# Kernel optimization log

Measured on AMD Instinct MI355X. Metric: run time of the kernel, lower is better.

## Reference

```python
import jax, jax.numpy as jnp
import numpy as np

N = 128          # batch size
C = 1000         # num_classes
NUM_DATA = 50000 # dataset size


def setup_inputs() -> dict:
    key = jax.random.key(0)
    k1, k2, k3 = jax.random.split(key, 3)
    outputs = jax.random.normal(k1, (N, C), dtype=jnp.float32)
    # label_confidence = train_givenY / rowsum(train_givenY): rows sum to 1
    conf = jax.random.uniform(k2, (NUM_DATA, C), dtype=jnp.float32)
    conf = conf / conf.sum(axis=1, keepdims=True)
    index = jax.random.randint(k3, (N,), 0, NUM_DATA, dtype=jnp.int64)
    return {"outputs": outputs, "label_confidence": conf, "index": index}


def reference(outputs, label_confidence, index):
    # softmax over classes: [N, C]
    p = jax.nn.softmax(outputs, axis=1)
    eye = jnp.eye(C, dtype=p.dtype)
    # |softmax broadcast vs one-hot|, summed over last dim -> [N, C]
    # (materializes [N, C, C] like the torch original)
    loss = jnp.abs(p[:, None, :] - eye[None, :, :]).sum(axis=-1)
    conf = label_confidence[index]          # [N, C]
    return (loss * conf).sum(axis=1).mean()
```

## Files before the change

kernel.cpp:

```cpp
#include <hip/hip_runtime.h>


#define NROWS 128
#define NCLS  1000

__global__ __launch_bounds__(256) void row_loss_kernel(
    const float* __restrict__ outputs,
    const float* __restrict__ conf,
    const int*   __restrict__ index,
    float* __restrict__ ws)
{
    const int row  = blockIdx.x;
    const int tid  = threadIdx.x;
    const int lane = tid & 63;
    const int wave = tid >> 6;

    __shared__ float redm[4];
    __shared__ float rz[4], rd[4], rs[4];
    __shared__ float bmax;

    const int j = tid * 4;
    float4 o = make_float4(-INFINITY, -INFINITY, -INFINITY, -INFINITY);
    if (j < NCLS) {
        o = *reinterpret_cast<const float4*>(outputs + (size_t)row * NCLS + j);
    }

    float m = fmaxf(fmaxf(o.x, o.y), fmaxf(o.z, o.w));
    #pragma unroll
    for (int off = 32; off > 0; off >>= 1)
        m = fmaxf(m, __shfl_down(m, off, 64));
    if (lane == 0) redm[wave] = m;
    __syncthreads();
    if (tid == 0)
        bmax = fmaxf(fmaxf(redm[0], redm[1]), fmaxf(redm[2], redm[3]));
    __syncthreads();
    m = bmax;

    float z = 0.f, dot = 0.f, sc = 0.f;
    if (j < NCLS) {
        const float* crow = conf + (size_t)index[row] * NCLS;
        const float4 cf = *reinterpret_cast<const float4*>(crow + j);
        const float e0 = __expf(o.x - m);
        const float e1 = __expf(o.y - m);
        const float e2 = __expf(o.z - m);
        const float e3 = __expf(o.w - m);
        z   = (e0 + e1) + (e2 + e3);
        dot = e0 * cf.x + e1 * cf.y + e2 * cf.z + e3 * cf.w;
        sc  = (cf.x + cf.y) + (cf.z + cf.w);
    }
    #pragma unroll
    for (int off = 32; off > 0; off >>= 1) {
        z   += __shfl_down(z,   off, 64);
        dot += __shfl_down(dot, off, 64);
        sc  += __shfl_down(sc,  off, 64);
    }
    if (lane == 0) { rz[wave] = z; rd[wave] = dot; rs[wave] = sc; }
    __syncthreads();
    if (tid == 0) {
        const float Z = (rz[0] + rz[1]) + (rz[2] + rz[3]);
        const float D = (rd[0] + rd[1]) + (rd[2] + rd[3]);
        const float S = (rs[0] + rs[1]) + (rs[2] + rs[3]);
        ws[row] = 2.f * S - 2.f * D / Z;
    }
}

__global__ __launch_bounds__(128) void final_reduce_kernel(
    const float* __restrict__ ws, float* __restrict__ out)
{
    const int tid = threadIdx.x;
    float v = ws[tid];
    #pragma unroll
    for (int off = 32; off > 0; off >>= 1)
        v += __shfl_down(v, off, 64);
    __shared__ float r[2];
    if ((tid & 63) == 0) r[tid >> 6] = v;
    __syncthreads();
    if (tid == 0) out[0] = (r[0] + r[1]) * (1.0f / (float)NROWS);
}

extern "C" void kernel_launch(void* const* d_in, const int* in_sizes, int n_in,
                              void* d_out, int out_size, void* d_ws, size_t ws_size,
                              hipStream_t stream) {
    const float* outputs = (const float*)d_in[0];
    const float* conf    = (const float*)d_in[1];
    const int*   index   = (const int*)d_in[2];
    float* out = (float*)d_out;
    float* ws  = (float*)d_ws;

    row_loss_kernel<<<NROWS, 256, 0, stream>>>(outputs, conf, index, ws);
    final_reduce_kernel<<<1, 128, 0, stream>>>(ws, out);
}
```

Before: 229.4 us.

## Fuse row loss and final reduction into a single-block wave-per-row kernel

Replaces the two-kernel design (128 blocks computing per-row loss, then a reduction kernel) with one 1024-thread block in which each wave processes eight rows using wave-level xor shuffles, then reduces per-wave sums in shared memory. This removes the second launch, the workspace round trip and the block-level barriers for row max. In exchange, all work runs on a single CU, so memory bandwidth and latency hiding are limited to one compute unit for roughly 1 MB of reads.

Result: slower. 249.0 us (+8.6%).

```diff
diff --git a/kernel.cpp b/kernel.cpp
--- a/kernel.cpp
+++ b/kernel.cpp
@@ -3,79 +3,82 @@
 
 #define NROWS 128
 #define NCLS  1000
+#define NF4   250
 
-__global__ __launch_bounds__(256) void row_loss_kernel(
+__global__ __launch_bounds__(1024) void fused_loss_kernel(
     const float* __restrict__ outputs,
     const float* __restrict__ conf,
     const int*   __restrict__ index,
-    float* __restrict__ ws)
+    float* __restrict__ out)
 {
-    const int row  = blockIdx.x;
     const int tid  = threadIdx.x;
     const int lane = tid & 63;
     const int wave = tid >> 6;
 
-    __shared__ float redm[4];
-    __shared__ float rz[4], rd[4], rs[4];
-    __shared__ float bmax;
+    int idxs[8];
+    #pragma unroll
+    for (int i = 0; i < 8; ++i) idxs[i] = index[wave + 16 * i];
 
-    const int j = tid * 4;
-    float4 o = make_float4(-INFINITY, -INFINITY, -INFINITY, -INFINITY);
-    if (j < NCLS) {
-        o = *reinterpret_cast<const float4*>(outputs + (size_t)row * NCLS + j);
+    float acc = 0.f;
+
+    #pragma unroll
+    for (int i = 0; i < 8; ++i) {
+        const int row = wave + 16 * i;
+        const float* orow = outputs + (size_t)row * NCLS;
+        const float* crow = conf + (size_t)idxs[i] * NCLS;
+
+        float4 o[4], c[4];
+        #pragma unroll
+        for (int k = 0; k < 4; ++k) {
+            const int p = lane + 64 * k;
+            o[k] = (p < NF4) ? reinterpret_cast<const float4*>(orow)[p]
+                             : make_float4(-INFINITY, -INFINITY, -INFINITY, -INFINITY);
+        }
+        #pragma unroll
+        for (int k = 0; k < 4; ++k) {
+            const int p = lane + 64 * k;
+            c[k] = (p < NF4) ? reinterpret_cast<const float4*>(crow)[p]
+                             : make_float4(0.f, 0.f, 0.f, 0.f);
+        }
+
+        float m = -INFINITY;
+        #pragma unroll
+        for (int k = 0; k < 4; ++k)
+            m = fmaxf(m, fmaxf(fmaxf(o[k].x, o[k].y), fmaxf(o[k].z, o[k].w)));
+        #pragma unroll
+        for (int off = 1; off < 64; off <<= 1)
+            m = fmaxf(m, __shfl_xor(m, off, 64));
+
+        float z = 0.f, dot = 0.f, sc = 0.f;
+        #pragma unroll
+        for (int k = 0; k < 4; ++k) {
+            const float e0 = __expf(o[k].x - m);
+            const float e1 = __expf(o[k].y - m);
+            const float e2 = __expf(o[k].z - m);
+            const float e3 = __expf(o[k].w - m);
+            z   += (e0 + e1) + (e2 + e3);
+            dot += e0 * c[k].x + e1 * c[k].y + e2 * c[k].z + e3 * c[k].w;
+            sc  += (c[k].x + c[k].y) + (c[k].z + c[k].w);
+        }
+        #pragma unroll
+        for (int off = 1; off < 64; off <<= 1) {
+            z   += __shfl_xor(z,   off, 64);
+            dot += __shfl_xor(dot, off, 64);
+            sc  += __shfl_xor(sc,  off, 64);
+        }
+
+        acc += 2.f * sc - 2.f * dot * __frcp_rn(z);
     }
 
-    float m = fmaxf(fmaxf(o.x, o.y), fmaxf(o.z, o.w));
-    #pragma unroll
-    for (int off = 32; off > 0; off >>= 1)
-        m = fmaxf(m, __shfl_down(m, off, 64));
-    if (lane == 0) redm[wave] = m;
-    __syncthreads();
-    if (tid == 0)
-        bmax = fmaxf(fmaxf(redm[0], redm[1]), fmaxf(redm[2], redm[3]));
-    __syncthreads();
-    m = bmax;
-
-    float z = 0.f, dot = 0.f, sc = 0.f;
-    if (j < NCLS) {
-        const float* crow = conf + (size_t)index[row] * NCLS;
-        const float4 cf = *reinterpret_cast<const float4*>(crow + j);
-        const float e0 = __expf(o.x - m);
-        const float e1 = __expf(o.y - m);
-        const float e2 = __expf(o.z - m);
-        const float e3 = __expf(o.w - m);
-        z   = (e0 + e1) + (e2 + e3);
-        dot = e0 * cf.x + e1 * cf.y + e2 * cf.z + e3 * cf.w;
-        sc  = (cf.x + cf.y) + (cf.z + cf.w);
-    }
-    #pragma unroll
-    for (int off = 32; off > 0; off >>= 1) {
-        z   += __shfl_down(z,   off, 64);
-        dot += __shfl_down(dot, off, 64);
-        sc  += __shfl_down(sc,  off, 64);
-    }
-    if (lane == 0) { rz[wave] = z; rd[wave] = dot; rs[wave] = sc; }
+    __shared__ float r[16];
+    if (lane == 0) r[wave] = acc;
     __syncthreads();
     if (tid == 0) {
-        const float Z = (rz[0] + rz[1]) + (rz[2] + rz[3]);
-        const float D = (rd[0] + rd[1]) + (rd[2] + rd[3]);
-        const float S = (rs[0] + rs[1]) + (rs[2] + rs[3]);
-        ws[row] = 2.f * S - 2.f * D / Z;
+        float t = 0.f;
+        #pragma unroll
+        for (int w = 0; w < 16; ++w) t += r[w];
+        out[0] = t * (1.0f / (float)NROWS);
     }
-}
-
-__global__ __launch_bounds__(128) void final_reduce_kernel(
-    const float* __restrict__ ws, float* __restrict__ out)
-{
-    const int tid = threadIdx.x;
-    float v = ws[tid];
-    #pragma unroll
-    for (int off = 32; off > 0; off >>= 1)
-        v += __shfl_down(v, off, 64);
-    __shared__ float r[2];
-    if ((tid & 63) == 0) r[tid >> 6] = v;
-    __syncthreads();
-    if (tid == 0) out[0] = (r[0] + r[1]) * (1.0f / (float)NROWS);
 }
 
 extern "C" void kernel_launch(void* const* d_in, const int* in_sizes, int n_in,
@@ -85,8 +88,6 @@
     const float* conf    = (const float*)d_in[1];
     const int*   index   = (const int*)d_in[2];
     float* out = (float*)d_out;
-    float* ws  = (float*)d_ws;
 
-    row_loss_kernel<<<NROWS, 256, 0, stream>>>(outputs, conf, index, ws);
-    final_reduce_kernel<<<1, 128, 0, stream>>>(ws, out);
+    fused_loss_kernel<<<1, 1024, 0, stream>>>(outputs, conf, index, out);
 }
```
